# Performance work log

Hardware: AMD Instinct MI355X
Metric: run time of the kernel (lower is better)

## Reference

```python
import jax, jax.numpy as jnp
import numpy as np

D_MODEL = 1024
NHEAD = 16
HEAD_DIM = D_MODEL // NHEAD
LN_EPS = 1e-5


def setup_inputs() -> dict:
    key = jax.random.key(0)
    ks = jax.random.split(key, 6)
    B, S = 4, 4096
    x = jax.random.normal(ks[0], (B, S, D_MODEL), dtype=jnp.float32)
    scale = 0.02
    Wq = jax.random.normal(ks[1], (D_MODEL, D_MODEL), dtype=jnp.float32) * scale
    Wv = jax.random.normal(ks[2], (D_MODEL, D_MODEL), dtype=jnp.float32) * scale
    Wo = jax.random.normal(ks[3], (D_MODEL, D_MODEL), dtype=jnp.float32) * scale
    Wg = jax.random.normal(ks[4], (D_MODEL, D_MODEL), dtype=jnp.float32) * scale
    beta = jnp.full((NHEAD,), -0.2, dtype=jnp.float32)
    ln_gamma = jnp.ones((D_MODEL,), dtype=jnp.float32)
    ln_beta = jnp.zeros((D_MODEL,), dtype=jnp.float32)
    return {"x": x, "Wq": Wq, "Wv": Wv, "Wo": Wo, "Wg": Wg,
            "beta": beta, "ln_gamma": ln_gamma, "ln_beta": ln_beta}


def _ema_scan(lam, v):
    # v: [B, S, H, D]; lam: [1, 1, H, 1]
    # s_t = lam * s_{t-1} + v_t, computed with a parallel associative scan
    # on pairs (a, b) representing the affine map s -> a*s + b.
    a = jnp.broadcast_to(lam, v.shape)

    def combine(e1, e2):
        a1, b1 = e1
        a2, b2 = e2
        return a1 * a2, a2 * b1 + b2

    _, state = jax.lax.associative_scan(combine, (a, v), axis=1)
    return state


def reference(x, Wq, Wv, Wo, Wg, beta, ln_gamma, ln_beta):
    B, S, _ = x.shape
    q = (x @ Wq.T).reshape(B, S, NHEAD, HEAD_DIM)
    v = (x @ Wv.T).reshape(B, S, NHEAD, HEAD_DIM)
    lam = jax.nn.sigmoid(beta).reshape(1, 1, NHEAD, 1).astype(v.dtype)
    state = _ema_scan(lam, v)                      # [B, S, H, D]
    y = (q * state).reshape(B, S, D_MODEL)
    # LayerNorm over last dim
    mu = jnp.mean(y, axis=-1, keepdims=True)
    var = jnp.mean(jnp.square(y - mu), axis=-1, keepdims=True)
    y = (y - mu) * jax.lax.rsqrt(var + LN_EPS) * ln_gamma + ln_beta
    gate = jax.nn.silu(x @ Wg.T)
    y = y * gate
    return y @ Wo.T
```

## Files before the change

kernel.cpp:

```cpp
#include <hip/hip_runtime.h>

#define D_MODEL 1024
#define NHEAD 16
#define LN_EPS 1e-5f
#define CHUNK 32
#define S_LEN 4096

typedef unsigned short u16;
typedef __attribute__((ext_vector_type(8))) short short8;
typedef __attribute__((ext_vector_type(4))) float f32x4;

__device__ __forceinline__ u16 f2b(float f) {
  unsigned u = __builtin_bit_cast(unsigned, f);
  u += 0x7FFFu + ((u >> 16) & 1u);
  return (u16)(u >> 16);
}
__device__ __forceinline__ float b2f(u16 s) {
  return __builtin_bit_cast(float, ((unsigned)s) << 16);
}

__device__ __forceinline__ ushort4 cvt4(float4 f) {
  ushort4 o; o.x = f2b(f.x); o.y = f2b(f.y); o.z = f2b(f.z); o.w = f2b(f.w);
  return o;
}
__global__ __launch_bounds__(256) void cvt_all(
    const float4* __restrict__ x,  const float4* __restrict__ wq,
    const float4* __restrict__ wv, const float4* __restrict__ wg,
    const float4* __restrict__ wo, ushort4* __restrict__ xb,
    ushort4* __restrict__ wqvg, ushort4* __restrict__ wob,
    const float* __restrict__ beta, float* __restrict__ lam,
    int nx4, int nw4) {
  int i = blockIdx.x * blockDim.x + threadIdx.x;
  int stride = gridDim.x * blockDim.x;
  if (blockIdx.x == 0 && threadIdx.x < NHEAD) {
    float l = 1.f / (1.f + __expf(-beta[threadIdx.x]));
    lam[threadIdx.x] = l;
    lam[NHEAD + threadIdx.x] = __log2f(l);
  }
  for (int j = i; j < nx4; j += stride) xb[j] = cvt4(x[j]);
  for (int j = i; j < nw4; j += stride) wqvg[j] = cvt4(wq[j]);
  for (int j = i; j < nw4; j += stride) wqvg[nw4 + j] = cvt4(wv[j]);
  for (int j = i; j < nw4; j += stride) wqvg[2 * nw4 + j] = cvt4(wg[j]);
  for (int j = i; j < nw4; j += stride) wob[j] = cvt4(wo[j]);
}


__device__ __forceinline__ void glds16(const u16* g, const u16* l) {
  __builtin_amdgcn_global_load_lds(
      (const __attribute__((address_space(1))) unsigned*)g,
      (__attribute__((address_space(3))) unsigned*)l, 16, 0, 0);
}

#define BAR() asm volatile("s_barrier" ::: "memory")
#define SB0() __builtin_amdgcn_sched_barrier(0)

template <typename OutT>
__global__ __launch_bounds__(512, 2) void gemm256(const u16* __restrict__ X,
                                                  const u16* __restrict__ W,
                                                  OutT* __restrict__ Out,
                                                  int M, int N, int K) {
  __shared__ u16 sm[8][8192];
  const int tid = threadIdx.x;
  const int lane = tid & 63;
  const int wave = tid >> 6;
  const int ln15 = lane & 15, lh = lane >> 4;
  const int wr = wave >> 2, wc = wave & 3;
  const int bm = blockIdx.x * 256, bn = blockIdx.y * 256;
  const int NT = K >> 6;

  const int srow = tid >> 3;
  const int scol = ((tid & 7) ^ (srow & 7)) << 3;
  const u16* Asrc = X + (size_t)(bm + srow) * K + scol;
  const u16* Bsrc = W + (size_t)(bn + srow) * K + scol;
  const int ldsw = wave * 512;

#define STAGE(u, h, tile, src)                                          \
  { const u16* _g = (src) + (size_t)((h) * 128) * K + (tile) * 64;      \
    glds16(_g,                  &sm[u][ldsw]);                          \
    glds16(_g + (size_t)64 * K, &sm[u][ldsw + 4096]); }

  const char* smb = (const char*)&sm[0][0];
  const char* Ard = smb + wr * 16384 + ln15 * 128;
  const char* Brd = smb + (2 + (wc >> 1)) * 16384 + ((wc & 1) * 64 + ln15) * 128;
  const int swz0 = ((lh ^ (ln15 & 7)) << 4);
  const int swz1 = (((4 + lh) ^ (ln15 & 7)) << 4);

#define RD_A(DB, MM, S) (*(const short8*)(Ard + (DB) + (MM) * 2048 + (S)))
#define RD_B(DB, NN, S) (*(const short8*)(Brd + (DB) + (NN) * 2048 + (S)))

  f32x4 acc[8][4];
  f32x4 zero = {0.f, 0.f, 0.f, 0.f};
  #pragma unroll
  for (int m = 0; m < 8; ++m)
    #pragma unroll
    for (int n = 0; n < 4; ++n) acc[m][n] = zero;

  short8 a[8][2], b[4][2];

#define MFMA_Q(M0, N0)                                                        \
  SB0();                                                                      \
  __builtin_amdgcn_s_setprio(1);                                              \
  _Pragma("unroll")                                                           \
  for (int m = (M0); m < (M0) + 4; ++m)                                       \
    _Pragma("unroll")                                                         \
    for (int n = (N0); n < (N0) + 2; ++n) {                                   \
      acc[m][n] = __builtin_amdgcn_mfma_f32_16x16x32_bf16(a[m][0], b[n][0], acc[m][n], 0, 0, 0); \
      acc[m][n] = __builtin_amdgcn_mfma_f32_16x16x32_bf16(a[m][1], b[n][1], acc[m][n], 0, 0, 0); \
    }                                                                         \
  __builtin_amdgcn_s_setprio(0);                                              \
  SB0();

  STAGE(0, 0, 0, Asrc); STAGE(1, 1, 0, Asrc);
  STAGE(2, 0, 0, Bsrc); STAGE(3, 1, 0, Bsrc);
  STAGE(4, 0, 1, Asrc); STAGE(5, 1, 1, Asrc);
  asm volatile("s_waitcnt vmcnt(4)" ::: "memory");
  BAR();
  #pragma unroll
  for (int m = 0; m < 4; ++m) { a[m][0] = RD_A(0, m, swz0); a[m][1] = RD_A(0, m, swz1); }
  #pragma unroll
  for (int n = 0; n < 4; ++n) { b[n][0] = RD_B(0, n, swz0); b[n][1] = RD_B(0, n, swz1); }

  for (int t = 0; t < NT; ++t) {
    const int d = t & 1;
    const int db = d * 65536;
    const int odb = (d ^ 1) * 65536;
    const int od = (d ^ 1) * 4;
    const int sd = d * 4;
    const int tB = (t + 1 < NT) ? t + 1 : NT - 1;
    const int tA = (t + 2 < NT) ? t + 2 : NT - 1;

    a[4][0] = RD_A(db, 4, swz0); a[4][1] = RD_A(db, 4, swz1);
    a[5][0] = RD_A(db, 5, swz0); a[5][1] = RD_A(db, 5, swz1);
    STAGE(od + 2, 0, tB, Bsrc);
    MFMA_Q(0, 0)

    a[6][0] = RD_A(db, 6, swz0); a[6][1] = RD_A(db, 6, swz1);
    a[7][0] = RD_A(db, 7, swz0); a[7][1] = RD_A(db, 7, swz1);
    STAGE(od + 3, 1, tB, Bsrc);
    MFMA_Q(0, 2)
    asm volatile("s_waitcnt vmcnt(4)" ::: "memory");
    BAR();

    #pragma unroll
    for (int m = 0; m < 4; ++m) { a[m][0] = RD_A(odb, m, swz0); a[m][1] = RD_A(odb, m, swz1); }
    MFMA_Q(4, 2)
    STAGE(sd + 0, 0, tA, Asrc);
    asm volatile("s_waitcnt vmcnt(2)" ::: "memory");
    BAR();

    b[2][0] = RD_B(odb, 2, swz0); b[2][1] = RD_B(odb, 2, swz1);
    b[3][0] = RD_B(odb, 3, swz0); b[3][1] = RD_B(odb, 3, swz1);
    MFMA_Q(4, 0)
    b[0][0] = RD_B(odb, 0, swz0); b[0][1] = RD_B(odb, 0, swz1);
    b[1][0] = RD_B(odb, 1, swz0); b[1][1] = RD_B(odb, 1, swz1);
    STAGE(sd + 1, 1, tA, Asrc);
  }
#undef STAGE
#undef RD_A
#undef RD_B
#undef MFMA_Q

  #pragma unroll
  for (int m = 0; m < 8; ++m)
    #pragma unroll
    for (int n = 0; n < 4; ++n)
      #pragma unroll
      for (int r = 0; r < 4; ++r) {
        int row = bm + wr * 128 + m * 16 + lh * 4 + r;
        int col = bn + wc * 64 + n * 16 + ln15;
        float vv = acc[m][n][r];
        if constexpr (sizeof(OutT) == 2) Out[(size_t)row * N + col] = f2b(vv);
        else                             Out[(size_t)row * N + col] = vv;
      }
}

__global__ __launch_bounds__(256) void scan_local(u16* __restrict__ v,
                                                  float* __restrict__ carry,
                                                  const float* __restrict__ lam,
                                                  int S, int nch, int ld) {
  int bj = blockIdx.x;
  int b = bj / nch, j = bj - b * nch;
  int col0 = threadIdx.x * 4;
  float l = lam[col0 >> 6];
  float s0 = 0.f, s1 = 0.f, s2 = 0.f, s3 = 0.f;
  size_t base = ((size_t)b * S + (size_t)j * CHUNK) * ld + col0;
  #pragma unroll 4
  for (int t = 0; t < CHUNK; ++t) {
    ushort4* p = (ushort4*)(v + base + (size_t)t * ld);
    ushort4 u = *p;
    s0 = l * s0 + b2f(u.x);
    s1 = l * s1 + b2f(u.y);
    s2 = l * s2 + b2f(u.z);
    s3 = l * s3 + b2f(u.w);
    u.x = f2b(s0); u.y = f2b(s1); u.z = f2b(s2); u.w = f2b(s3);
    *p = u;
  }
  size_t cb = (size_t)bj * D_MODEL + col0;
  carry[cb] = s0; carry[cb + 1] = s1; carry[cb + 2] = s2; carry[cb + 3] = s3;
}

__global__ void scan_carry(float* __restrict__ carry, const float* __restrict__ lam,
                           int B, int nch) {
  int idx = blockIdx.x * blockDim.x + threadIdx.x;
  if (idx >= B * D_MODEL) return;
  int b = idx >> 10, col = idx & (D_MODEL - 1);
  float lC = exp2f(lam[NHEAD + (col >> 6)] * (float)CHUNK);
  float c = 0.f;
  #pragma unroll 4
  for (int j = 0; j < nch; ++j) {
    size_t a = ((size_t)(b * nch + j)) * D_MODEL + col;
    c = lC * c + carry[a];
    carry[a] = c;
  }
}

__global__ __launch_bounds__(256) void ew_ln(const u16* __restrict__ qvg,
    const float* __restrict__ carry, const float* __restrict__ lam,
    const float* __restrict__ gamma, const float* __restrict__ lbeta,
    u16* __restrict__ yout, int S, int nch, int ld) {
  int row = blockIdx.x;
  int b = row / S, s = row - b * S;
  int j = s / CHUNK, tl = s - j * CHUNK;
  int tid = threadIdx.x;
  int col0 = tid * 4;
  size_t rb = (size_t)row * ld;

  ushort4 qu = *(const ushort4*)(qvg + rb + col0);
  ushort4 su = *(const ushort4*)(qvg + rb + D_MODEL + col0);
  float st[4] = {b2f(su.x), b2f(su.y), b2f(su.z), b2f(su.w)};
  if (j > 0) {
    float p = exp2f(lam[NHEAD + (col0 >> 6)] * (float)(tl + 1));
    const float4 c4 = *(const float4*)(carry + ((size_t)(b * nch + j - 1)) * D_MODEL + col0);
    st[0] += p * c4.x; st[1] += p * c4.y; st[2] += p * c4.z; st[3] += p * c4.w;
  }
  float q[4] = {b2f(qu.x), b2f(qu.y), b2f(qu.z), b2f(qu.w)};
  float y[4];
  float sum = 0.f, sumsq = 0.f;
  #pragma unroll
  for (int i = 0; i < 4; ++i) {
    y[i] = q[i] * st[i];
    sum += y[i];
    sumsq += y[i] * y[i];
  }
  #pragma unroll
  for (int off = 32; off > 0; off >>= 1) {
    sum += __shfl_down(sum, off);
    sumsq += __shfl_down(sumsq, off);
  }
  __shared__ float red[8];
  int ln = tid & 63, wv = tid >> 6;
  if (ln == 0) { red[wv] = sum; red[4 + wv] = sumsq; }
  __syncthreads();
  sum = red[0] + red[1] + red[2] + red[3];
  sumsq = red[4] + red[5] + red[6] + red[7];
  float mu = sum * (1.f / 1024.f);
  float var = sumsq * (1.f / 1024.f) - mu * mu;
  float rstd = rsqrtf(var + LN_EPS);

  float4 gm = *(const float4*)(gamma + col0);
  float4 bt = *(const float4*)(lbeta + col0);
  ushort4 gu = *(const ushort4*)(qvg + rb + 2 * D_MODEL + col0);
  float gv[4]  = {b2f(gu.x), b2f(gu.y), b2f(gu.z), b2f(gu.w)};
  float gmv[4] = {gm.x, gm.y, gm.z, gm.w};
  float btv[4] = {bt.x, bt.y, bt.z, bt.w};
  u16 ov[4];
  #pragma unroll
  for (int i = 0; i < 4; ++i) {
    float gate = gv[i] / (1.f + __expf(-gv[i]));
    float oo = ((y[i] - mu) * rstd * gmv[i] + btv[i]) * gate;
    ov[i] = f2b(oo);
  }
  ushort4 o; o.x = ov[0]; o.y = ov[1]; o.z = ov[2]; o.w = ov[3];
  *(ushort4*)(yout + (size_t)row * D_MODEL + col0) = o;
}

extern "C" void kernel_launch(void* const* d_in, const int* in_sizes, int n_in,
                              void* d_out, int out_size, void* d_ws, size_t ws_size,
                              hipStream_t stream) {
  const float* x     = (const float*)d_in[0];
  const float* Wq    = (const float*)d_in[1];
  const float* Wv    = (const float*)d_in[2];
  const float* Wo    = (const float*)d_in[3];
  const float* Wg    = (const float*)d_in[4];
  const float* beta  = (const float*)d_in[5];
  const float* gamma = (const float*)d_in[6];
  const float* lbeta = (const float*)d_in[7];
  float* out = (float*)d_out;

  const int BS = in_sizes[0] / D_MODEL;
  const int S = S_LEN;
  const int B = BS / S;
  const int nch = S / CHUNK;
  const size_t nx = (size_t)BS * D_MODEL;
  const size_t nw = (size_t)D_MODEL * D_MODEL;
  const int N3 = 3 * D_MODEL;

  char* w = (char*)d_ws;
  u16* xb   = (u16*)w;  w += nx * 2;
  u16* wqvg = (u16*)w;  w += 3 * nw * 2;
  u16* wob  = (u16*)w;  w += nw * 2;
  u16* qvg  = (u16*)w;  w += (size_t)BS * N3 * 2;
  u16* yb   = (u16*)w;  w += nx * 2;
  float* carry = (float*)w;  w += (size_t)B * nch * D_MODEL * 4;
  float* lam = (float*)w;

  cvt_all<<<2048, 256, 0, stream>>>((const float4*)x, (const float4*)Wq,
      (const float4*)Wv, (const float4*)Wg, (const float4*)Wo,
      (ushort4*)xb, (ushort4*)wqvg, (ushort4*)wob, beta, lam,
      (int)(nx / 4), (int)(nw / 4));

  dim3 g1(BS / 256, N3 / 256);
  gemm256<u16><<<g1, 512, 0, stream>>>(xb, wqvg, qvg, BS, N3, D_MODEL);

  scan_local<<<B * nch, 256, 0, stream>>>(qvg + D_MODEL, carry, lam, S, nch, N3);
  scan_carry<<<(B * D_MODEL + 255) / 256, 256, 0, stream>>>(carry, lam, B, nch);
  ew_ln<<<BS, 256, 0, stream>>>(qvg, carry, lam, gamma, lbeta, yb, S, nch, N3);

  dim3 g2(BS / 256, D_MODEL / 256);
  gemm256<float><<<g2, 512, 0, stream>>>(yb, wob, out, BS, D_MODEL, D_MODEL);
}
```

Measured before the change: 237.9 us.

## Fuse chunk carry computation into QVG GEMM epilogue and merge scan with LayerNorm

The QVG GEMM epilogue now computes each 32-row chunk's end-of-chunk EMA carry for the V columns as a weighted sum of accumulator rows with lambda powers, using wave shuffles. This removes the separate scan_local kernel and its read-modify-write of V. The per-row ew_ln kernel becomes a per-chunk scan_ln kernel that runs the local recurrence sequentially over 32 rows, adds the propagated carry, and applies LayerNorm and gating row by row. The trade is fewer launches and less V traffic against a serial loop with a block barrier on every row and fewer blocks in flight.

```diff
diff --git a/kernel.cpp b/kernel.cpp
--- a/kernel.cpp
+++ b/kernel.cpp
@@ -5,6 +5,7 @@
 #define LN_EPS 1e-5f
 #define CHUNK 32
 #define S_LEN 4096
+#define NCH (S_LEN / CHUNK)
 
 typedef unsigned short u16;
 typedef __attribute__((ext_vector_type(8))) short short8;
@@ -54,10 +55,12 @@
 #define BAR() asm volatile("s_barrier" ::: "memory")
 #define SB0() __builtin_amdgcn_sched_barrier(0)
 
-template <typename OutT>
+template <typename OutT, bool CARRY>
 __global__ __launch_bounds__(512, 2) void gemm256(const u16* __restrict__ X,
                                                   const u16* __restrict__ W,
                                                   OutT* __restrict__ Out,
+                                                  float* __restrict__ carry,
+                                                  const float* __restrict__ lamlog,
                                                   int M, int N, int K) {
   __shared__ u16 sm[8][8192];
   const int tid = threadIdx.x;
@@ -172,31 +175,38 @@
         if constexpr (sizeof(OutT) == 2) Out[(size_t)row * N + col] = f2b(vv);
         else                             Out[(size_t)row * N + col] = vv;
       }
-}
-
-__global__ __launch_bounds__(256) void scan_local(u16* __restrict__ v,
-                                                  float* __restrict__ carry,
-                                                  const float* __restrict__ lam,
-                                                  int S, int nch, int ld) {
-  int bj = blockIdx.x;
-  int b = bj / nch, j = bj - b * nch;
-  int col0 = threadIdx.x * 4;
-  float l = lam[col0 >> 6];
-  float s0 = 0.f, s1 = 0.f, s2 = 0.f, s3 = 0.f;
-  size_t base = ((size_t)b * S + (size_t)j * CHUNK) * ld + col0;
-  #pragma unroll 4
-  for (int t = 0; t < CHUNK; ++t) {
-    ushort4* p = (ushort4*)(v + base + (size_t)t * ld);
-    ushort4 u = *p;
-    s0 = l * s0 + b2f(u.x);
-    s1 = l * s1 + b2f(u.y);
-    s2 = l * s2 + b2f(u.z);
-    s3 = l * s3 + b2f(u.w);
-    u.x = f2b(s0); u.y = f2b(s1); u.z = f2b(s2); u.w = f2b(s3);
-    *p = u;
-  }
-  size_t cb = (size_t)bj * D_MODEL + col0;
-  carry[cb] = s0; carry[cb + 1] = s1; carry[cb + 2] = s2; carry[cb + 3] = s3;
+
+  if constexpr (CARRY) {
+    if (bn >= 1024 && bn < 2048) {
+      const int bidx = bm >> 12;
+      const int chunkbase = ((bm & 4095) >> 5) + wr * 4;
+      const int colbase = (bn - 1024) + wc * 64;
+      const float l2h = lamlog[colbase >> 6];
+      float wgt[2][4];
+      #pragma unroll
+      for (int mo = 0; mo < 2; ++mo)
+        #pragma unroll
+        for (int r = 0; r < 4; ++r)
+          wgt[mo][r] = exp2f(l2h * (float)(31 - (mo * 16 + lh * 4 + r)));
+      #pragma unroll
+      for (int mq = 0; mq < 4; ++mq) {
+        #pragma unroll
+        for (int n = 0; n < 4; ++n) {
+          float part = 0.f;
+          #pragma unroll
+          for (int mo = 0; mo < 2; ++mo)
+            #pragma unroll
+            for (int r = 0; r < 4; ++r)
+              part += wgt[mo][r] * acc[mq * 2 + mo][n][r];
+          part += __shfl_down(part, 16);
+          part += __shfl_down(part, 32);
+          if (lh == 0)
+            carry[(size_t)(bidx * NCH + chunkbase + mq) * D_MODEL +
+                  colbase + n * 16 + ln15] = part;
+        }
+      }
+    }
+  }
 }
 
 __global__ void scan_carry(float* __restrict__ carry, const float* __restrict__ lam,
@@ -214,64 +224,78 @@
   }
 }
 
-__global__ __launch_bounds__(256) void ew_ln(const u16* __restrict__ qvg,
+__global__ __launch_bounds__(256) void scan_ln(const u16* __restrict__ qvg,
     const float* __restrict__ carry, const float* __restrict__ lam,
     const float* __restrict__ gamma, const float* __restrict__ lbeta,
     u16* __restrict__ yout, int S, int nch, int ld) {
-  int row = blockIdx.x;
-  int b = row / S, s = row - b * S;
-  int j = s / CHUNK, tl = s - j * CHUNK;
-  int tid = threadIdx.x;
-  int col0 = tid * 4;
-  size_t rb = (size_t)row * ld;
-
-  ushort4 qu = *(const ushort4*)(qvg + rb + col0);
-  ushort4 su = *(const ushort4*)(qvg + rb + D_MODEL + col0);
-  float st[4] = {b2f(su.x), b2f(su.y), b2f(su.z), b2f(su.w)};
+  const int bj = blockIdx.x;
+  const int b = bj / nch, j = bj - b * nch;
+  const int tid = threadIdx.x;
+  const int col0 = tid * 4;
+  const float l = lam[col0 >> 6];
+  const float4 gm = *(const float4*)(gamma + col0);
+  const float4 bt = *(const float4*)(lbeta + col0);
+
+  float cp0 = 0.f, cp1 = 0.f, cp2 = 0.f, cp3 = 0.f;
   if (j > 0) {
-    float p = exp2f(lam[NHEAD + (col0 >> 6)] * (float)(tl + 1));
-    const float4 c4 = *(const float4*)(carry + ((size_t)(b * nch + j - 1)) * D_MODEL + col0);
-    st[0] += p * c4.x; st[1] += p * c4.y; st[2] += p * c4.z; st[3] += p * c4.w;
-  }
-  float q[4] = {b2f(qu.x), b2f(qu.y), b2f(qu.z), b2f(qu.w)};
-  float y[4];
-  float sum = 0.f, sumsq = 0.f;
-  #pragma unroll
-  for (int i = 0; i < 4; ++i) {
-    y[i] = q[i] * st[i];
-    sum += y[i];
-    sumsq += y[i] * y[i];
-  }
-  #pragma unroll
-  for (int off = 32; off > 0; off >>= 1) {
-    sum += __shfl_down(sum, off);
-    sumsq += __shfl_down(sumsq, off);
-  }
-  __shared__ float red[8];
-  int ln = tid & 63, wv = tid >> 6;
-  if (ln == 0) { red[wv] = sum; red[4 + wv] = sumsq; }
-  __syncthreads();
-  sum = red[0] + red[1] + red[2] + red[3];
-  sumsq = red[4] + red[5] + red[6] + red[7];
-  float mu = sum * (1.f / 1024.f);
-  float var = sumsq * (1.f / 1024.f) - mu * mu;
-  float rstd = rsqrtf(var + LN_EPS);
-
-  float4 gm = *(const float4*)(gamma + col0);
-  float4 bt = *(const float4*)(lbeta + col0);
-  ushort4 gu = *(const ushort4*)(qvg + rb + 2 * D_MODEL + col0);
-  float gv[4]  = {b2f(gu.x), b2f(gu.y), b2f(gu.z), b2f(gu.w)};
-  float gmv[4] = {gm.x, gm.y, gm.z, gm.w};
-  float btv[4] = {bt.x, bt.y, bt.z, bt.w};
-  u16 ov[4];
-  #pragma unroll
-  for (int i = 0; i < 4; ++i) {
-    float gate = gv[i] / (1.f + __expf(-gv[i]));
-    float oo = ((y[i] - mu) * rstd * gmv[i] + btv[i]) * gate;
-    ov[i] = f2b(oo);
-  }
-  ushort4 o; o.x = ov[0]; o.y = ov[1]; o.z = ov[2]; o.w = ov[3];
-  *(ushort4*)(yout + (size_t)row * D_MODEL + col0) = o;
+    const float4 c4 = *(const float4*)(carry + (size_t)(bj - 1) * D_MODEL + col0);
+    cp0 = c4.x; cp1 = c4.y; cp2 = c4.z; cp3 = c4.w;
+  }
+  float p = l;
+  float s0 = 0.f, s1 = 0.f, s2 = 0.f, s3 = 0.f;
+  const size_t row0 = (size_t)b * S + (size_t)j * CHUNK;
+  const size_t rb0 = row0 * ld;
+
+  ushort4 qu = *(const ushort4*)(qvg + rb0 + col0);
+  ushort4 su = *(const ushort4*)(qvg + rb0 + D_MODEL + col0);
+  ushort4 gu = *(const ushort4*)(qvg + rb0 + 2 * D_MODEL + col0);
+
+  __shared__ float red[2][8];
+  const int ln = tid & 63, wv = tid >> 6;
+
+  for (int t = 0; t < CHUNK; ++t) {
+    ushort4 qn, sn, gn;
+    if (t + 1 < CHUNK) {
+      size_t nb = rb0 + (size_t)(t + 1) * ld;
+      qn = *(const ushort4*)(qvg + nb + col0);
+      sn = *(const ushort4*)(qvg + nb + D_MODEL + col0);
+      gn = *(const ushort4*)(qvg + nb + 2 * D_MODEL + col0);
+    }
+    s0 = l * s0 + b2f(su.x);
+    s1 = l * s1 + b2f(su.y);
+    s2 = l * s2 + b2f(su.z);
+    s3 = l * s3 + b2f(su.w);
+    float st0 = s0 + p * cp0, st1 = s1 + p * cp1;
+    float st2 = s2 + p * cp2, st3 = s3 + p * cp3;
+    float y0 = b2f(qu.x) * st0, y1 = b2f(qu.y) * st1;
+    float y2 = b2f(qu.z) * st2, y3 = b2f(qu.w) * st3;
+    float sum = y0 + y1 + y2 + y3;
+    float sumsq = y0 * y0 + y1 * y1 + y2 * y2 + y3 * y3;
+    #pragma unroll
+    for (int off = 32; off > 0; off >>= 1) {
+      sum += __shfl_down(sum, off);
+      sumsq += __shfl_down(sumsq, off);
+    }
+    const int par = t & 1;
+    if (ln == 0) { red[par][wv] = sum; red[par][4 + wv] = sumsq; }
+    __syncthreads();
+    sum = red[par][0] + red[par][1] + red[par][2] + red[par][3];
+    sumsq = red[par][4] + red[par][5] + red[par][6] + red[par][7];
+    float mu = sum * (1.f / 1024.f);
+    float var = sumsq * (1.f / 1024.f) - mu * mu;
+    float rstd = rsqrtf(var + LN_EPS);
+
+    float g0 = b2f(gu.x), g1 = b2f(gu.y), g2 = b2f(gu.z), g3 = b2f(gu.w);
+    float o0 = ((y0 - mu) * rstd * gm.x + bt.x) * (g0 / (1.f + __expf(-g0)));
+    float o1 = ((y1 - mu) * rstd * gm.y + bt.y) * (g1 / (1.f + __expf(-g1)));
+    float o2 = ((y2 - mu) * rstd * gm.z + bt.z) * (g2 / (1.f + __expf(-g2)));
+    float o3 = ((y3 - mu) * rstd * gm.w + bt.w) * (g3 / (1.f + __expf(-g3)));
+    ushort4 o; o.x = f2b(o0); o.y = f2b(o1); o.z = f2b(o2); o.w = f2b(o3);
+    *(ushort4*)(yout + (row0 + t) * D_MODEL + col0) = o;
+
+    if (t + 1 < CHUNK) { qu = qn; su = sn; gu = gn; }
+    p *= l;
+  }
 }
 
 extern "C" void kernel_launch(void* const* d_in, const int* in_sizes, int n_in,
@@ -290,7 +314,7 @@
   const int BS = in_sizes[0] / D_MODEL;
   const int S = S_LEN;
   const int B = BS / S;
-  const int nch = S / CHUNK;
+  const int nch = NCH;
   const size_t nx = (size_t)BS * D_MODEL;
   const size_t nw = (size_t)D_MODEL * D_MODEL;
   const int N3 = 3 * D_MODEL;
@@ -310,12 +334,13 @@
       (int)(nx / 4), (int)(nw / 4));
 
   dim3 g1(BS / 256, N3 / 256);
-  gemm256<u16><<<g1, 512, 0, stream>>>(xb, wqvg, qvg, BS, N3, D_MODEL);
-
-  scan_local<<<B * nch, 256, 0, stream>>>(qvg + D_MODEL, carry, lam, S, nch, N3);
+  gemm256<u16, true><<<g1, 512, 0, stream>>>(xb, wqvg, qvg, carry, lam + NHEAD,
+                                             BS, N3, D_MODEL);
+
   scan_carry<<<(B * D_MODEL + 255) / 256, 256, 0, stream>>>(carry, lam, B, nch);
-  ew_ln<<<BS, 256, 0, stream>>>(qvg, carry, lam, gamma, lbeta, yb, S, nch, N3);
+  scan_ln<<<B * nch, 256, 0, stream>>>(qvg, carry, lam, gamma, lbeta, yb, S, nch, N3);
 
   dim3 g2(BS / 256, D_MODEL / 256);
-  gemm256<float><<<g2, 512, 0, stream>>>(yb, wob, out, BS, D_MODEL, D_MODEL);
-}
+  gemm256<float, false><<<g2, 512, 0, stream>>>(yb, wob, out, nullptr, nullptr,
+                                                BS, D_MODEL, D_MODEL);
+}
```

After: 224.7 us. 1.06x faster.

## Fuse intra-chunk EMA scan into QVG GEMM epilogue via register shuffles

Applied to the files above, without the earlier changes.

Removes the separate scan_local kernel. The QVG GEMM epilogue now computes the 32-row chunk-local EMA scan directly on the MFMA accumulator registers for the V columns, using in-register prefix steps and wave shuffles across the 16-lane groups. Chunk-end states are written to the carry buffer from the epilogue. This avoids a full read-modify-write pass over V in bf16 and one kernel launch. In exchange it adds shuffle and ALU work to the GEMM epilogue for a third of its tiles, and the scan now runs in fp32 before rounding to bf16.

```diff
diff --git a/kernel.cpp b/kernel.cpp
--- a/kernel.cpp
+++ b/kernel.cpp
@@ -5,6 +5,7 @@
 #define LN_EPS 1e-5f
 #define CHUNK 32
 #define S_LEN 4096
+#define NCH (S_LEN / CHUNK)
 
 typedef unsigned short u16;
 typedef __attribute__((ext_vector_type(8))) short short8;
@@ -54,10 +55,12 @@
 #define BAR() asm volatile("s_barrier" ::: "memory")
 #define SB0() __builtin_amdgcn_sched_barrier(0)
 
-template <typename OutT>
+template <typename OutT, bool CARRY>
 __global__ __launch_bounds__(512, 2) void gemm256(const u16* __restrict__ X,
                                                   const u16* __restrict__ W,
                                                   OutT* __restrict__ Out,
+                                                  float* __restrict__ carry,
+                                                  const float* __restrict__ lamlog,
                                                   int M, int N, int K) {
   __shared__ u16 sm[8][8192];
   const int tid = threadIdx.x;
@@ -160,6 +163,37 @@
 #undef RD_B
 #undef MFMA_Q
 
+  if constexpr (CARRY) {
+    if (bn >= 1024 && bn < 2048) {
+      const float l2h = lamlog[((bn - 1024) + wc * 64) >> 6];
+      const float lp1 = exp2f(l2h);
+      const float lp2 = lp1 * lp1, lp3 = lp2 * lp1, lp4 = lp2 * lp2;
+      const float l8 = lp4 * lp4;
+      const float lpl = exp2f(l2h * (float)(4 * lh));
+      #pragma unroll
+      for (int q = 0; q < 4; ++q)
+        #pragma unroll
+        for (int n = 0; n < 4; ++n) {
+          f32x4 A0 = acc[2 * q][n], A1 = acc[2 * q + 1][n];
+          A0[1] += lp1 * A0[0]; A0[2] += lp1 * A0[1]; A0[3] += lp1 * A0[2];
+          A1[1] += lp1 * A1[0]; A1[2] += lp1 * A1[1]; A1[3] += lp1 * A1[2];
+          float S = A0[3], x;
+          x = __shfl_up(S, 16); if (lh >= 1) S += lp4 * x;
+          x = __shfl_up(S, 32); if (lh >= 2) S += l8 * x;
+          float Xc = __shfl_up(S, 16); Xc = (lh >= 1) ? Xc : 0.f;
+          A0[0] += lp1 * Xc; A0[1] += lp2 * Xc; A0[2] += lp3 * Xc; A0[3] += lp4 * Xc;
+          float f15 = __shfl(A0[3], 48 + ln15);
+          S = A1[3];
+          x = __shfl_up(S, 16); if (lh >= 1) S += lp4 * x;
+          x = __shfl_up(S, 32); if (lh >= 2) S += l8 * x;
+          Xc = __shfl_up(S, 16); Xc = (lh >= 1) ? Xc : 0.f;
+          Xc += lpl * f15;
+          A1[0] += lp1 * Xc; A1[1] += lp2 * Xc; A1[2] += lp3 * Xc; A1[3] += lp4 * Xc;
+          acc[2 * q][n] = A0; acc[2 * q + 1][n] = A1;
+        }
+    }
+  }
+
   #pragma unroll
   for (int m = 0; m < 8; ++m)
     #pragma unroll
@@ -172,31 +206,20 @@
         if constexpr (sizeof(OutT) == 2) Out[(size_t)row * N + col] = f2b(vv);
         else                             Out[(size_t)row * N + col] = vv;
       }
-}
-
-__global__ __launch_bounds__(256) void scan_local(u16* __restrict__ v,
-                                                  float* __restrict__ carry,
-                                                  const float* __restrict__ lam,
-                                                  int S, int nch, int ld) {
-  int bj = blockIdx.x;
-  int b = bj / nch, j = bj - b * nch;
-  int col0 = threadIdx.x * 4;
-  float l = lam[col0 >> 6];
-  float s0 = 0.f, s1 = 0.f, s2 = 0.f, s3 = 0.f;
-  size_t base = ((size_t)b * S + (size_t)j * CHUNK) * ld + col0;
-  #pragma unroll 4
-  for (int t = 0; t < CHUNK; ++t) {
-    ushort4* p = (ushort4*)(v + base + (size_t)t * ld);
-    ushort4 u = *p;
-    s0 = l * s0 + b2f(u.x);
-    s1 = l * s1 + b2f(u.y);
-    s2 = l * s2 + b2f(u.z);
-    s3 = l * s3 + b2f(u.w);
-    u.x = f2b(s0); u.y = f2b(s1); u.z = f2b(s2); u.w = f2b(s3);
-    *p = u;
-  }
-  size_t cb = (size_t)bj * D_MODEL + col0;
-  carry[cb] = s0; carry[cb + 1] = s1; carry[cb + 2] = s2; carry[cb + 3] = s3;
+
+  if constexpr (CARRY) {
+    if (bn >= 1024 && bn < 2048 && lh == 3) {
+      const int bidx = bm >> 12;
+      const int chunkbase = ((bm & 4095) >> 5) + wr * 4;
+      const int colbase = (bn - 1024) + wc * 64;
+      #pragma unroll
+      for (int q = 0; q < 4; ++q)
+        #pragma unroll
+        for (int n = 0; n < 4; ++n)
+          carry[(size_t)(bidx * NCH + chunkbase + q) * D_MODEL +
+                colbase + n * 16 + ln15] = acc[2 * q + 1][n][3];
+    }
+  }
 }
 
 __global__ void scan_carry(float* __restrict__ carry, const float* __restrict__ lam,
@@ -217,10 +240,11 @@
 __global__ __launch_bounds__(256) void ew_ln(const u16* __restrict__ qvg,
     const float* __restrict__ carry, const float* __restrict__ lam,
     const float* __restrict__ gamma, const float* __restrict__ lbeta,
-    u16* __restrict__ yout, int S, int nch, int ld) {
+    u16* __restrict__ yout, int nch, int ld) {
   int row = blockIdx.x;
-  int b = row / S, s = row - b * S;
-  int j = s / CHUNK, tl = s - j * CHUNK;
+  int b = row >> 12;
+  int srow = row & 4095;
+  int j = srow >> 5, tl = srow & 31;
   int tid = threadIdx.x;
   int col0 = tid * 4;
   size_t rb = (size_t)row * ld;
@@ -288,9 +312,8 @@
   float* out = (float*)d_out;
 
   const int BS = in_sizes[0] / D_MODEL;
-  const int S = S_LEN;
-  const int B = BS / S;
-  const int nch = S / CHUNK;
+  const int B = BS / S_LEN;
+  const int nch = NCH;
   const size_t nx = (size_t)BS * D_MODEL;
   const size_t nw = (size_t)D_MODEL * D_MODEL;
   const int N3 = 3 * D_MODEL;
@@ -310,12 +333,13 @@
       (int)(nx / 4), (int)(nw / 4));
 
   dim3 g1(BS / 256, N3 / 256);
-  gemm256<u16><<<g1, 512, 0, stream>>>(xb, wqvg, qvg, BS, N3, D_MODEL);
-
-  scan_local<<<B * nch, 256, 0, stream>>>(qvg + D_MODEL, carry, lam, S, nch, N3);
+  gemm256<u16, true><<<g1, 512, 0, stream>>>(xb, wqvg, qvg, carry, lam + NHEAD,
+                                             BS, N3, D_MODEL);
+
   scan_carry<<<(B * D_MODEL + 255) / 256, 256, 0, stream>>>(carry, lam, B, nch);
-  ew_ln<<<BS, 256, 0, stream>>>(qvg, carry, lam, gamma, lbeta, yb, S, nch, N3);
+  ew_ln<<<BS, 256, 0, stream>>>(qvg, carry, lam, gamma, lbeta, yb, nch, N3);
 
   dim3 g2(BS / 256, D_MODEL / 256);
-  gemm256<float><<<g2, 512, 0, stream>>>(yb, wob, out, BS, D_MODEL, D_MODEL);
-}
+  gemm256<float, false><<<g2, 512, 0, stream>>>(yb, wob, out, nullptr, nullptr,
+                                                BS, D_MODEL, D_MODEL);
+}
```

New measurement: 223.4 us, median of 3. 6.1% less time.
